# Kernel tuning notes

Measured on AMD Instinct MI355X. Metric: run time of the kernel, lower is better.

Reference implementation:

```python
import jax, jax.numpy as jnp
import numpy as np

N_NODES = 10000
N_EDGES = 320000
D_IN = 256
D_OUT = 256
MAX_NORM = 0.95

def setup_inputs() -> dict:
    key = jax.random.key(0)
    ks = jax.random.split(key, 7)
    x = jax.random.normal(ks[0], (N_NODES, D_IN), dtype=jnp.float32)
    edge_index = jax.random.randint(ks[1], (2, N_EDGES), 0, N_NODES, dtype=jnp.int64)
    # xavier-ish scales
    W = jax.random.normal(ks[2], (D_OUT, D_IN), dtype=jnp.float32) * (1.0 / np.sqrt(D_IN))
    b = jax.random.normal(ks[3], (D_OUT,), dtype=jnp.float32) * 0.02
    mag_w = jax.random.normal(ks[4], (1, D_IN), dtype=jnp.float32) * 0.02
    mag_b = jax.random.normal(ks[5], (1,), dtype=jnp.float32) * 0.02
    attn_w = jax.random.normal(ks[6], (1, 2 * D_OUT), dtype=jnp.float32) * (1.0 / np.sqrt(2 * D_OUT))
    return {"x": x, "edge_index": edge_index, "W": W, "b": b,
            "mag_w": mag_w, "mag_b": mag_b, "attn_w": attn_w}

def _expmap0(u):
    # Poincare ball exp map at origin, curvature c = 1.0
    un = jnp.linalg.norm(u, axis=-1, keepdims=True)
    un_c = jnp.maximum(un, 1e-15)
    return jnp.tanh(un_c) * u / un_c

def reference(x, edge_index, W, b, mag_w, mag_b, attn_w):
    N = x.shape[0]
    F_out = W.shape[0]
    # linear transform + directional/magnitude decomposition
    h_raw = x @ W.T + b                                              # (N, F)
    h_dir = h_raw / jnp.maximum(jnp.linalg.norm(h_raw, axis=-1, keepdims=True), 1e-12)
    h_mag = jax.nn.sigmoid(x @ mag_w.T + mag_b) * 1.5                # (N, 1)
    h = h_dir * h_mag                                                # (N, F)
    src, tgt = edge_index[0], edge_index[1]
    h_src = h[src]                                                   # (E, F)
    h_tgt = h[tgt]                                                   # (E, F)
    # attn(cat([h_src, h_tgt])) == h_src @ a_s + h_tgt @ a_t (avoids concat)
    a_s, a_t = attn_w[0, :F_out], attn_w[0, F_out:]
    scores = h_src @ a_s + h_tgt @ a_t                               # (E,)
    # scatter softmax over edges grouped by target node
    mx = jnp.maximum(jax.ops.segment_max(scores, tgt, num_segments=N), -1e9)
    ex = jnp.exp(scores - mx[tgt])
    se = jax.ops.segment_sum(ex, tgt, num_segments=N)
    attn_weights = ex / (se[tgt] + 1e-10)                            # (E,)
    # weighted message aggregation
    agg = jax.ops.segment_sum(h_src * attn_weights[:, None], tgt, num_segments=N)
    h_combined = h + agg
    h_poincare = _expmap0(h_combined)
    norms = jnp.linalg.norm(h_poincare, axis=1, keepdims=True)
    return jnp.where(norms > MAX_NORM, h_poincare * (MAX_NORM / (norms + 1e-8)), h_poincare)
```

## Files before the change

### kernel.cpp

```cpp
#include <hip/hip_runtime.h>
#include <math.h>

#define N_NODES 10000
#define N_EDGES 320000
#define D 256
#define HALF (N_NODES / 2)
#define CAP_H 64
#define BM 32
#define LDK 40
#define GB_GEMM ((N_NODES + BM - 1) / BM)
#define GB_BUILD ((N_EDGES + 255) / 256)

typedef __attribute__((ext_vector_type(8))) short short8;
typedef __attribute__((ext_vector_type(4))) float f32x4;

__device__ __forceinline__ ushort f2bf(float f) {
    union { float f; unsigned u; } v; v.f = f;
    unsigned r = v.u + 0x7FFFu + ((v.u >> 16) & 1u);
    return (ushort)(r >> 16);
}
__device__ __forceinline__ float bf2f(ushort u) {
    union { unsigned u; float f; } v; v.u = (unsigned)u << 16;
    return v.f;
}

__global__ __launch_bounds__(256) void k_prep(const float* __restrict__ W,
                                              ushort* __restrict__ Wb,
                                              unsigned* __restrict__ deg) {
    const int tid = blockIdx.x * 256 + threadIdx.x;
    const int i = tid * 4;
    const float4 v = *(const float4*)&W[i];
    ushort4 o;
    o.x = f2bf(v.x); o.y = f2bf(v.y); o.z = f2bf(v.z); o.w = f2bf(v.w);
    *(ushort4*)&Wb[i] = o;
    for (int j = tid; j < 2 * N_NODES; j += (D * D) / 4) deg[j] = 0u;
}

__global__ __launch_bounds__(256) void k_main(const float* __restrict__ x,
                                              const ushort* __restrict__ Wb,
                                              const float* __restrict__ b,
                                              const float* __restrict__ mag_w,
                                              const float* __restrict__ mag_b,
                                              const float* __restrict__ attn_w,
                                              const int* __restrict__ ei,
                                              unsigned* __restrict__ deg,
                                              int* __restrict__ csr,
                                              ushort* __restrict__ hb,
                                              float* __restrict__ es) {
    if (blockIdx.x >= GB_GEMM) {
        const int e = (blockIdx.x - GB_GEMM) * 256 + threadIdx.x;
        if (e < N_EDGES) {
            int src = ei[e];
            int tgt = ei[N_EDGES + e];
            src = min(max(src, 0), N_NODES - 1);
            tgt = min(max(tgt, 0), N_NODES - 1);
            const int half = (src >= HALF);
            const unsigned slot = atomicAdd(&deg[tgt + half * N_NODES], 1u);
            if (slot < CAP_H)
                csr[((size_t)tgt * 2 + half) * CAP_H + slot] = src;
        }
        return;
    }

    __shared__ ushort ldsA[2][BM * LDK];
    __shared__ ushort ldsB[2][256 * LDK];
    __shared__ float red_ssq[4][BM], red_ra[4][BM];
    __shared__ float smrow[BM], scl[BM];

    const int t = threadIdx.x;
    const int w = t >> 6, l = t & 63;
    const int bm = blockIdx.x * BM;
    const int sra = t >> 3, ka = (t & 7) * 4;
    const int am = bm + sra;
    const int srb = t >> 2, kb = (t & 3) * 8;
    const int fl = l & 15;
    const int fh = (l >> 4) * 8;
    const int rq = (l >> 4) * 4;

    f32x4 acc[2][4];
#pragma unroll
    for (int r = 0; r < 2; ++r)
#pragma unroll
        for (int c = 0; c < 4; ++c) acc[r][c] = (f32x4)(0.f);
    float sm_part = 0.f;

    float4 xa;
    short8 bv[4];

    {
        xa = make_float4(0.f, 0.f, 0.f, 0.f);
        if (am < N_NODES) xa = *(const float4*)&x[(size_t)am * D + ka];
        const float4 mwv = *(const float4*)&mag_w[ka];
        sm_part += xa.x * mwv.x + xa.y * mwv.y + xa.z * mwv.z + xa.w * mwv.w;
#pragma unroll
        for (int p = 0; p < 4; ++p)
            bv[p] = *(const short8*)&Wb[(size_t)(p * 64 + srb) * D + kb];
        ushort4 av;
        av.x = f2bf(xa.x); av.y = f2bf(xa.y); av.z = f2bf(xa.z); av.w = f2bf(xa.w);
        *(ushort4*)&ldsA[0][sra * LDK + ka] = av;
#pragma unroll
        for (int p = 0; p < 4; ++p)
            *(short8*)&ldsB[0][(p * 64 + srb) * LDK + kb] = bv[p];
    }
    __syncthreads();

    int cur = 0;
    for (int k0 = 32; k0 < D; k0 += 32) {
        xa = make_float4(0.f, 0.f, 0.f, 0.f);
        if (am < N_NODES) xa = *(const float4*)&x[(size_t)am * D + k0 + ka];
        const float4 mwv = *(const float4*)&mag_w[k0 + ka];
        sm_part += xa.x * mwv.x + xa.y * mwv.y + xa.z * mwv.z + xa.w * mwv.w;
#pragma unroll
        for (int p = 0; p < 4; ++p)
            bv[p] = *(const short8*)&Wb[(size_t)(p * 64 + srb) * D + k0 + kb];

        short8 af[2], bfr[4];
#pragma unroll
        for (int r = 0; r < 2; ++r)
            af[r] = *(short8*)&ldsA[cur][(r * 16 + fl) * LDK + fh];
#pragma unroll
        for (int c = 0; c < 4; ++c)
            bfr[c] = *(short8*)&ldsB[cur][(w * 64 + c * 16 + fl) * LDK + fh];
#pragma unroll
        for (int r = 0; r < 2; ++r)
#pragma unroll
            for (int c = 0; c < 4; ++c)
                acc[r][c] = __builtin_amdgcn_mfma_f32_16x16x32_bf16(af[r], bfr[c], acc[r][c], 0, 0, 0);

        ushort4 av;
        av.x = f2bf(xa.x); av.y = f2bf(xa.y); av.z = f2bf(xa.z); av.w = f2bf(xa.w);
        *(ushort4*)&ldsA[cur ^ 1][sra * LDK + ka] = av;
#pragma unroll
        for (int p = 0; p < 4; ++p)
            *(short8*)&ldsB[cur ^ 1][(p * 64 + srb) * LDK + kb] = bv[p];
        __syncthreads();
        cur ^= 1;
    }
    {
        short8 af[2], bfr[4];
#pragma unroll
        for (int r = 0; r < 2; ++r)
            af[r] = *(short8*)&ldsA[cur][(r * 16 + fl) * LDK + fh];
#pragma unroll
        for (int c = 0; c < 4; ++c)
            bfr[c] = *(short8*)&ldsB[cur][(w * 64 + c * 16 + fl) * LDK + fh];
#pragma unroll
        for (int r = 0; r < 2; ++r)
#pragma unroll
            for (int c = 0; c < 4; ++c)
                acc[r][c] = __builtin_amdgcn_mfma_f32_16x16x32_bf16(af[r], bfr[c], acc[r][c], 0, 0, 0);
    }

#pragma unroll
    for (int o = 1; o < 8; o <<= 1) sm_part += __shfl_xor(sm_part, o);
    if ((t & 7) == 0) smrow[sra] = sm_part;

    float bn[4], asn[4];
#pragma unroll
    for (int c = 0; c < 4; ++c) {
        const int n = w * 64 + c * 16 + fl;
        bn[c]  = b[n];
        asn[c] = attn_w[n];
    }

#pragma unroll
    for (int r = 0; r < 2; ++r) {
#pragma unroll
        for (int reg = 0; reg < 4; ++reg) {
            float vssq = 0.f, vra = 0.f;
#pragma unroll
            for (int c = 0; c < 4; ++c) {
                const float v = acc[r][c][reg] + bn[c];
                vssq += v * v;
                vra  += v * asn[c];
            }
#pragma unroll
            for (int o = 1; o < 16; o <<= 1) {
                vssq += __shfl_xor(vssq, o);
                vra  += __shfl_xor(vra, o);
            }
            if (fl == 0) {
                const int m = r * 16 + rq + reg;
                red_ssq[w][m] = vssq;
                red_ra[w][m]  = vra;
            }
        }
    }
    __syncthreads();

    if (t < BM) {
        const int gm = bm + t;
        const float ssq = red_ssq[0][t] + red_ssq[1][t] + red_ssq[2][t] + red_ssq[3][t];
        const float ra  = red_ra[0][t]  + red_ra[1][t]  + red_ra[2][t]  + red_ra[3][t];
        const float norm = sqrtf(ssq);
        const float mag  = 1.5f / (1.f + expf(-(smrow[t] + mag_b[0])));
        const float scale = mag / fmaxf(norm, 1e-12f);
        scl[t] = scale;
        if (gm < N_NODES) es[gm] = expf(ra * scale);
    }
    __syncthreads();

#pragma unroll
    for (int r = 0; r < 2; ++r) {
#pragma unroll
        for (int reg = 0; reg < 4; ++reg) {
            const int ml = r * 16 + rq + reg;
            const int m = bm + ml;
            if (m < N_NODES) {
                const float scale = scl[ml];
#pragma unroll
                for (int c = 0; c < 4; ++c) {
                    const int n = w * 64 + c * 16 + fl;
                    hb[(size_t)m * D + n] = f2bf((acc[r][c][reg] + bn[c]) * scale);
                }
            }
        }
    }
}

__global__ __launch_bounds__(256) void k_agg(const ushort* __restrict__ hb,
                                             const unsigned* __restrict__ deg,
                                             const int* __restrict__ csr,
                                             const float* __restrict__ es,
                                             float* __restrict__ out) {
    const int wv = threadIdx.x >> 6;
    const int n = blockIdx.x * 4 + wv;
    const int lane = threadIdx.x & 63;
    const int d0 = min((int)deg[n], CAP_H);
    const int d1 = min((int)deg[n + N_NODES], CAP_H);
    const size_t cbase = (size_t)n * 2 * CAP_H;

    int src0 = 0, src1 = 0;
    float w0 = 0.f, w1 = 0.f;
    if (lane < d0) { src0 = csr[cbase + lane];         w0 = es[src0]; }
    if (lane < d1) { src1 = csr[cbase + CAP_H + lane]; w1 = es[src1]; }
    float sum = w0 + w1;
#pragma unroll
    for (int o = 32; o > 0; o >>= 1) sum += __shfl_xor(sum, o);
    const float inv = 1.f / (sum + 1e-10f);

    const int coff = lane * 4;
    float4 A0 = make_float4(0.f, 0.f, 0.f, 0.f), A1 = A0, A2 = A0, A3 = A0;

#pragma unroll
    for (int pass = 0; pass < 2; ++pass) {
        const int cnt = pass ? d1 : d0;
        const int sreg = pass ? src1 : src0;
        const float wreg = pass ? w1 : w0;
        int e = 0;
        for (; e + 8 <= cnt; e += 8) {
            int s[8]; float q[8]; ushort4 v[8];
#pragma unroll
            for (int j = 0; j < 8; ++j) { s[j] = __shfl(sreg, e + j); q[j] = __shfl(wreg, e + j); }
#pragma unroll
            for (int j = 0; j < 8; ++j) v[j] = *(const ushort4*)&hb[(size_t)s[j] * D + coff];
#pragma unroll
            for (int j = 0; j < 8; ++j) {
                float4* A = (j & 2) ? ((j & 1) ? &A3 : &A2) : ((j & 1) ? &A1 : &A0);
                A->x += q[j] * bf2f(v[j].x); A->y += q[j] * bf2f(v[j].y);
                A->z += q[j] * bf2f(v[j].z); A->w += q[j] * bf2f(v[j].w);
            }
        }
        for (; e < cnt; ++e) {
            const int s0 = __shfl(sreg, e);
            const float q0 = __shfl(wreg, e);
            const ushort4 v0 = *(const ushort4*)&hb[(size_t)s0 * D + coff];
            A0.x += q0 * bf2f(v0.x); A0.y += q0 * bf2f(v0.y); A0.z += q0 * bf2f(v0.z); A0.w += q0 * bf2f(v0.w);
        }
    }
    float4 acc = make_float4((A0.x + A1.x + A2.x + A3.x) * inv,
                             (A0.y + A1.y + A2.y + A3.y) * inv,
                             (A0.z + A1.z + A2.z + A3.z) * inv,
                             (A0.w + A1.w + A2.w + A3.w) * inv);

    const ushort4 hnv = *(const ushort4*)&hb[(size_t)n * D + coff];
    float4 u = make_float4(bf2f(hnv.x) + acc.x, bf2f(hnv.y) + acc.y,
                           bf2f(hnv.z) + acc.z, bf2f(hnv.w) + acc.w);
    float ssq = u.x * u.x + u.y * u.y + u.z * u.z + u.w * u.w;
#pragma unroll
    for (int o = 32; o > 0; o >>= 1) ssq += __shfl_xor(ssq, o);
    const float un = sqrtf(ssq);
    const float un_c = fmaxf(un, 1e-15f);
    const float th = tanhf(un_c);
    float s = th / un_c;
    const float pn = th * (un / un_c);
    if (pn > 0.95f) s *= 0.95f / (pn + 1e-8f);
    float4 p = make_float4(u.x * s, u.y * s, u.z * s, u.w * s);
    *(float4*)&out[(size_t)n * D + coff] = p;
}

extern "C" void kernel_launch(void* const* d_in, const int* in_sizes, int n_in,
                              void* d_out, int out_size, void* d_ws, size_t ws_size,
                              hipStream_t stream) {
    const float* x      = (const float*)d_in[0];
    const int*   ei     = (const int*)d_in[1];
    const float* W      = (const float*)d_in[2];
    const float* b      = (const float*)d_in[3];
    const float* mag_w  = (const float*)d_in[4];
    const float* mag_b  = (const float*)d_in[5];
    const float* attn_w = (const float*)d_in[6];
    float* out = (float*)d_out;

    char* ws = (char*)d_ws;
    ushort* hb = (ushort*)ws;         ws += (size_t)N_NODES * D * sizeof(ushort);
    float* es = (float*)ws;           ws += (size_t)N_NODES * sizeof(float);
    unsigned* deg = (unsigned*)ws;    ws += (size_t)2 * N_NODES * sizeof(unsigned);
    int* csr = (int*)ws;              ws += (size_t)N_NODES * 2 * CAP_H * sizeof(int);
    ushort* Wb = (ushort*)ws;         ws += (size_t)D * D * sizeof(ushort);

    k_prep<<<(D * D) / (256 * 4), 256, 0, stream>>>(W, Wb, deg);
    k_main<<<GB_GEMM + GB_BUILD, 256, 0, stream>>>(
        x, Wb, b, mag_w, mag_b, attn_w, ei, deg, csr, hb, es);
    k_agg<<<N_NODES / 4, 256, 0, stream>>>(hb, deg, csr, es, out);
}
```

Before: 57.67 us.

## Fuse prep kernel into main via in-kernel gate and on-the-fly W conversion

Removes the separate k_prep launch. Block 0 of the fused kernel now zeroes the degree counters and releases a global gate flag. Edge-build blocks spin on that flag before their atomics, and k_agg resets it for the next call. GEMM blocks read fp32 W directly and convert it to bf16 while staging into LDS, which removes the Wb buffer but doubles W load bytes per block and adds conversion ALU work. The spin-wait relies on block 0 being scheduled and has a bounded timeout, so it carries a correctness and forward-progress risk if the gate is not seen.

```diff
diff --git a/kernel.cpp b/kernel.cpp
--- a/kernel.cpp
+++ b/kernel.cpp
@@ -10,6 +10,7 @@
 #define LDK 40
 #define GB_GEMM ((N_NODES + BM - 1) / BM)
 #define GB_BUILD ((N_EDGES + 255) / 256)
+#define MAGIC 0x7A11C0DEu
 
 typedef __attribute__((ext_vector_type(8))) short short8;
 typedef __attribute__((ext_vector_type(4))) float f32x4;
@@ -23,32 +24,47 @@
     union { unsigned u; float f; } v; v.u = (unsigned)u << 16;
     return v.f;
 }
-
-__global__ __launch_bounds__(256) void k_prep(const float* __restrict__ W,
-                                              ushort* __restrict__ Wb,
-                                              unsigned* __restrict__ deg) {
-    const int tid = blockIdx.x * 256 + threadIdx.x;
-    const int i = tid * 4;
-    const float4 v = *(const float4*)&W[i];
-    ushort4 o;
-    o.x = f2bf(v.x); o.y = f2bf(v.y); o.z = f2bf(v.z); o.w = f2bf(v.w);
-    *(ushort4*)&Wb[i] = o;
-    for (int j = tid; j < 2 * N_NODES; j += (D * D) / 4) deg[j] = 0u;
-}
-
-__global__ __launch_bounds__(256) void k_main(const float* __restrict__ x,
-                                              const ushort* __restrict__ Wb,
-                                              const float* __restrict__ b,
-                                              const float* __restrict__ mag_w,
-                                              const float* __restrict__ mag_b,
-                                              const float* __restrict__ attn_w,
-                                              const int* __restrict__ ei,
-                                              unsigned* __restrict__ deg,
-                                              int* __restrict__ csr,
-                                              ushort* __restrict__ hb,
-                                              float* __restrict__ es) {
-    if (blockIdx.x >= GB_GEMM) {
-        const int e = (blockIdx.x - GB_GEMM) * 256 + threadIdx.x;
+__device__ __forceinline__ short8 cvt8(const float4 a, const float4 b) {
+    short8 r;
+    r[0] = f2bf(a.x); r[1] = f2bf(a.y); r[2] = f2bf(a.z); r[3] = f2bf(a.w);
+    r[4] = f2bf(b.x); r[5] = f2bf(b.y); r[6] = f2bf(b.z); r[7] = f2bf(b.w);
+    return r;
+}
+
+__global__ __launch_bounds__(256) void k_front(const float* __restrict__ x,
+                                               const float* __restrict__ W,
+                                               const float* __restrict__ b,
+                                               const float* __restrict__ mag_w,
+                                               const float* __restrict__ mag_b,
+                                               const float* __restrict__ attn_w,
+                                               const int* __restrict__ ei,
+                                               unsigned* __restrict__ deg,
+                                               unsigned* __restrict__ gate,
+                                               int* __restrict__ csr,
+                                               ushort* __restrict__ hb,
+                                               float* __restrict__ es) {
+    const int t = threadIdx.x;
+    if (blockIdx.x == 0) {
+        uint4 z = make_uint4(0u, 0u, 0u, 0u);
+        for (int i = t; i < (2 * N_NODES) / 4; i += 256)
+            *(uint4*)&deg[i * 4] = z;
+        __threadfence();
+        __syncthreads();
+        if (t == 0)
+            __hip_atomic_store(gate, MAGIC, __ATOMIC_RELEASE, __HIP_MEMORY_SCOPE_AGENT);
+        return;
+    }
+    if (blockIdx.x > GB_GEMM) {
+        if (t == 0) {
+            int g = 0;
+            while (__hip_atomic_load(gate, __ATOMIC_ACQUIRE,
+                                     __HIP_MEMORY_SCOPE_AGENT) != MAGIC) {
+                __builtin_amdgcn_s_sleep(2);
+                if (++g > (1 << 20)) break;
+            }
+        }
+        __syncthreads();
+        const int e = (blockIdx.x - 1 - GB_GEMM) * 256 + t;
         if (e < N_EDGES) {
             int src = ei[e];
             int tgt = ei[N_EDGES + e];
@@ -67,9 +83,8 @@
     __shared__ float red_ssq[4][BM], red_ra[4][BM];
     __shared__ float smrow[BM], scl[BM];
 
-    const int t = threadIdx.x;
     const int w = t >> 6, l = t & 63;
-    const int bm = blockIdx.x * BM;
+    const int bm = (blockIdx.x - 1) * BM;
     const int sra = t >> 3, ka = (t & 7) * 4;
     const int am = bm + sra;
     const int srb = t >> 2, kb = (t & 3) * 8;
@@ -84,35 +99,37 @@
         for (int c = 0; c < 4; ++c) acc[r][c] = (f32x4)(0.f);
     float sm_part = 0.f;
 
-    float4 xa;
-    short8 bv[4];
-
     {
-        xa = make_float4(0.f, 0.f, 0.f, 0.f);
+        float4 xa = make_float4(0.f, 0.f, 0.f, 0.f);
         if (am < N_NODES) xa = *(const float4*)&x[(size_t)am * D + ka];
         const float4 mwv = *(const float4*)&mag_w[ka];
         sm_part += xa.x * mwv.x + xa.y * mwv.y + xa.z * mwv.z + xa.w * mwv.w;
-#pragma unroll
-        for (int p = 0; p < 4; ++p)
-            bv[p] = *(const short8*)&Wb[(size_t)(p * 64 + srb) * D + kb];
         ushort4 av;
         av.x = f2bf(xa.x); av.y = f2bf(xa.y); av.z = f2bf(xa.z); av.w = f2bf(xa.w);
         *(ushort4*)&ldsA[0][sra * LDK + ka] = av;
 #pragma unroll
-        for (int p = 0; p < 4; ++p)
-            *(short8*)&ldsB[0][(p * 64 + srb) * LDK + kb] = bv[p];
+        for (int p = 0; p < 4; ++p) {
+            const size_t row = (size_t)(p * 64 + srb) * D + kb;
+            const float4 w0 = *(const float4*)&W[row];
+            const float4 w1 = *(const float4*)&W[row + 4];
+            *(short8*)&ldsB[0][(p * 64 + srb) * LDK + kb] = cvt8(w0, w1);
+        }
     }
     __syncthreads();
 
     int cur = 0;
     for (int k0 = 32; k0 < D; k0 += 32) {
-        xa = make_float4(0.f, 0.f, 0.f, 0.f);
+        float4 xa = make_float4(0.f, 0.f, 0.f, 0.f);
         if (am < N_NODES) xa = *(const float4*)&x[(size_t)am * D + k0 + ka];
         const float4 mwv = *(const float4*)&mag_w[k0 + ka];
         sm_part += xa.x * mwv.x + xa.y * mwv.y + xa.z * mwv.z + xa.w * mwv.w;
-#pragma unroll
-        for (int p = 0; p < 4; ++p)
-            bv[p] = *(const short8*)&Wb[(size_t)(p * 64 + srb) * D + k0 + kb];
+        float4 wv[4][2];
+#pragma unroll
+        for (int p = 0; p < 4; ++p) {
+            const size_t row = (size_t)(p * 64 + srb) * D + k0 + kb;
+            wv[p][0] = *(const float4*)&W[row];
+            wv[p][1] = *(const float4*)&W[row + 4];
+        }
 
         short8 af[2], bfr[4];
 #pragma unroll
@@ -132,7 +149,7 @@
         *(ushort4*)&ldsA[cur ^ 1][sra * LDK + ka] = av;
 #pragma unroll
         for (int p = 0; p < 4; ++p)
-            *(short8*)&ldsB[cur ^ 1][(p * 64 + srb) * LDK + kb] = bv[p];
+            *(short8*)&ldsB[cur ^ 1][(p * 64 + srb) * LDK + kb] = cvt8(wv[p][0], wv[p][1]);
         __syncthreads();
         cur ^= 1;
     }
@@ -220,9 +237,13 @@
 
 __global__ __launch_bounds__(256) void k_agg(const ushort* __restrict__ hb,
                                              const unsigned* __restrict__ deg,
+                                             unsigned* __restrict__ gate,
                                              const int* __restrict__ csr,
                                              const float* __restrict__ es,
                                              float* __restrict__ out) {
+    if (blockIdx.x == 0 && threadIdx.x == 0)
+        __hip_atomic_store(gate, 0u, __ATOMIC_RELAXED, __HIP_MEMORY_SCOPE_AGENT);
+
     const int wv = threadIdx.x >> 6;
     const int n = blockIdx.x * 4 + wv;
     const int lane = threadIdx.x & 63;
@@ -306,10 +327,9 @@
     float* es = (float*)ws;           ws += (size_t)N_NODES * sizeof(float);
     unsigned* deg = (unsigned*)ws;    ws += (size_t)2 * N_NODES * sizeof(unsigned);
     int* csr = (int*)ws;              ws += (size_t)N_NODES * 2 * CAP_H * sizeof(int);
-    ushort* Wb = (ushort*)ws;         ws += (size_t)D * D * sizeof(ushort);
-
-    k_prep<<<(D * D) / (256 * 4), 256, 0, stream>>>(W, Wb, deg);
-    k_main<<<GB_GEMM + GB_BUILD, 256, 0, stream>>>(
-        x, Wb, b, mag_w, mag_b, attn_w, ei, deg, csr, hb, es);
-    k_agg<<<N_NODES / 4, 256, 0, stream>>>(hb, deg, csr, es, out);
-}
+    unsigned* gate = (unsigned*)ws;   ws += 256;
+
+    k_front<<<1 + GB_GEMM + GB_BUILD, 256, 0, stream>>>(
+        x, W, b, mag_w, mag_b, attn_w, ei, deg, gate, csr, hb, es);
+    k_agg<<<N_NODES / 4, 256, 0, stream>>>(hb, deg, gate, csr, es, out);
+}
```

After: 123.6 us. 2.14x slower.
